# Kernel optimization log

Measured on AMD Instinct MI355X. Metric: run time of the kernel, lower is better.

Reference implementation:

```python
import jax, jax.numpy as jnp
import numpy as np

H = 256  # hidden_size


def setup_inputs() -> dict:
    key = jax.random.key(0)
    k1, k2, k3 = jax.random.split(key, 3)
    N, L, V, Emb = 128, 2048, 32000, 256
    X = jax.random.randint(k1, (N, L), 0, V, dtype=jnp.int64)
    E = jax.random.normal(k2, (V, Emb), dtype=jnp.float32) * 0.02
    W_w = jax.random.normal(k3, (4 * H, H + Emb), dtype=jnp.float32) * (1.0 / np.sqrt(H + Emb))
    W_b = jnp.zeros((4 * H,), dtype=jnp.float32)
    return {"X": X, "E": E, "W_w": W_w, "W_b": W_b}


def reference(X, E, W_w, W_b):
    # X: (N, L) int token ids
    N, L = X.shape
    Xe = E[X]                      # (N, L, Emb) embedded sequence
    Xe_t = jnp.swapaxes(Xe, 0, 1)  # (L, N, Emb) scan over time

    def step(carry, x_t):
        H_t, C_t = carry
        hx = jnp.concatenate([H_t, x_t], axis=1)           # (N, H+Emb)
        G = hx @ W_w.T + W_b                               # (N, 4H)
        F_g = jax.nn.sigmoid(G[:, :H])
        # NOTE: original code computes I = sigmoid(G[:, H:2H]) but never uses it
        O_g = jax.nn.sigmoid(G[:, 2 * H:3 * H])
        H_tmp = jnp.tanh(G[:, 3 * H:4 * H])
        # Faithful to source: C_t = F*C + O*H_tmp (uses O, not I)
        C_new = F_g * C_t + O_g * H_tmp
        H_new = O_g * jnp.tanh(C_new)
        return (H_new, C_new), None

    init = (jnp.zeros((N, H), Xe.dtype), jnp.zeros((N, H), Xe.dtype))
    (H_last, _), _ = jax.lax.scan(step, init, Xe_t)
    return H_last
```

## Files before the change

### kernel.cpp

```cpp
#include <hip/hip_runtime.h>
#include <hip/hip_bf16.h>

#define N_B   128
#define L_SEQ 2048
#define H_DIM 256
#define EMB   256
#define G3    768
#define G4    1024
#define WROW  512
#define V_SZ  32000


typedef unsigned short ushort_t;
typedef unsigned int   uint_t;

using f32x4  = __attribute__((ext_vector_type(4))) float;
using bf16x8 = __attribute__((ext_vector_type(8))) short;
using h2_t   = __attribute__((ext_vector_type(2))) _Float16;
using f16x8  = __attribute__((ext_vector_type(8))) _Float16;
using ushort4_t = __attribute__((ext_vector_type(4))) ushort_t;
using u32x4  = __attribute__((ext_vector_type(4))) uint_t;

__device__ __forceinline__ float bf2f(ushort_t u) {
  union { uint_t u; float f; } x; x.u = ((uint_t)u) << 16; return x.f;
}
__device__ __forceinline__ ushort_t f2bf(float f) {
  union { float f; uint_t u; } x; x.f = f;
  return (ushort_t)((x.u + 0x7fffu + ((x.u >> 16) & 1u)) >> 16);
}
__device__ __forceinline__ float rcp_f(float x) {
#if __has_builtin(__builtin_amdgcn_rcpf)
  return __builtin_amdgcn_rcpf(x);
#else
  return 1.0f / x;
#endif
}
__device__ __forceinline__ float clampf(float x, float lo, float hi) {
  return fminf(fmaxf(x, lo), hi);
}
__device__ __forceinline__ float sigmoid_f(float x) {
  x = clampf(x, -30.f, 30.f);
  return rcp_f(1.0f + __expf(-x));
}
__device__ __forceinline__ float tanh_f(float x) {
  x = clampf(x, -15.f, 15.f);
  float e = __expf(-2.0f * x);
  return (1.0f - e) * rcp_f(1.0f + e);
}
__device__ __forceinline__ h2_t bfpair_to_h2(uint_t u) {
  union { uint_t u; float f; } lo, hi;
  lo.u = u << 16;
  hi.u = u & 0xffff0000u;
  h2_t r; r.x = (_Float16)lo.f; r.y = (_Float16)hi.f; return r;
}

__device__ __forceinline__ int gmap(int g) { return (g < 256) ? g : g + 256; }

#define FENCE_V8(A) asm volatile("" :                                         \
  "+v"((A)[0]), "+v"((A)[1]), "+v"((A)[2]), "+v"((A)[3]),                     \
  "+v"((A)[4]), "+v"((A)[5]), "+v"((A)[6]), "+v"((A)[7]))

__global__ void dtype_probe(const uint_t* __restrict__ Ed,
                            const uint_t* __restrict__ Xd,
                            const uint_t* __restrict__ Wd,
                            uint_t* __restrict__ flags) {
  if (threadIdx.x != 0 || blockIdx.x != 0) return;
  int saneE = 0, saneW = 0;
  for (int i = 0; i < 256; ++i) {
    uint_t le = Ed[i] & 0xffffu, ee = (le >> 7) & 0xffu;
    if (ee == 0u || (ee >= 90u && ee <= 126u)) saneE++;
    uint_t lw = Wd[i] & 0xffffu, ew = (lw >> 7) & 0xffu;
    if (ew == 0u || (ew >= 90u && ew <= 126u)) saneW++;
  }
  uint_t nz = 0u;
  for (int i = 0; i < 128; ++i) nz |= Xd[2 * i + 1];
  flags[0] = (saneE < 192) ? 1u : 0u;
  flags[1] = (nz == 0u) ? 1u : 0u;
  flags[2] = (saneW < 192) ? 1u : 0u;
}

__global__ __launch_bounds__(256) void eg_gemm(const void* __restrict__ Ein,
                                               const void* __restrict__ Wwin,
                                               const void* __restrict__ Wbin,
                                               _Float16* __restrict__ Eg,
                                               const uint_t* __restrict__ flags) {
  __shared__ __align__(16) ushort_t At[16][264];
  const int tid = threadIdx.x;
  const int v0  = blockIdx.x * 16;
  const uint_t ef32 = flags[0];
  const uint_t wf32 = flags[2];

  if (!ef32) {
    const ushort_t* E = (const ushort_t*)Ein;
#pragma unroll
    for (int i = 0; i < 2; ++i) {
      int idx = tid + i * 256;
      int row = idx >> 5, seg = idx & 31;
      const uint4* src = (const uint4*)(E + (size_t)(v0 + row) * EMB + seg * 8);
      *(uint4*)&At[row][seg * 8] = *src;
    }
  } else {
    const float* Ef = (const float*)Ein;
#pragma unroll
    for (int i = 0; i < 4; ++i) {
      int idx = tid + i * 256;
      int row = idx >> 6, seg = idx & 63;
      float4 v = *(const float4*)(Ef + (size_t)(v0 + row) * EMB + seg * 4);
      ushort4_t s;
      s.x = f2bf(v.x); s.y = f2bf(v.y); s.z = f2bf(v.z); s.w = f2bf(v.w);
      *(ushort4_t*)&At[row][seg * 4] = s;
    }
  }
  __syncthreads();

  const int lane = tid & 63, wv = tid >> 6;
  const int m = lane & 15, q = lane >> 4;

  f32x4 acc[12];
#pragma unroll
  for (int nt = 0; nt < 12; ++nt) acc[nt] = f32x4{0.f, 0.f, 0.f, 0.f};

  if (!wf32) {
    const ushort_t* Ww = (const ushort_t*)Wwin;
#pragma unroll
    for (int kt = 0; kt < 8; ++kt) {
      bf16x8 a = *(const bf16x8*)&At[m][kt * 32 + q * 8];
#pragma unroll
      for (int nt = 0; nt < 12; ++nt) {
        int g  = wv * 192 + nt * 16 + m;
        int gr = gmap(g);
        const bf16x8* bp =
            (const bf16x8*)(Ww + (size_t)gr * WROW + EMB + kt * 32 + q * 8);
        acc[nt] = __builtin_amdgcn_mfma_f32_16x16x32_bf16(a, *bp, acc[nt], 0, 0, 0);
      }
    }
  } else {
    const float* Wf = (const float*)Wwin;
#pragma unroll
    for (int kt = 0; kt < 8; ++kt) {
      bf16x8 a = *(const bf16x8*)&At[m][kt * 32 + q * 8];
#pragma unroll
      for (int nt = 0; nt < 12; ++nt) {
        int g  = wv * 192 + nt * 16 + m;
        int gr = gmap(g);
        const float* wp = Wf + (size_t)gr * WROW + EMB + kt * 32 + q * 8;
        float4 w0 = *(const float4*)(wp);
        float4 w1 = *(const float4*)(wp + 4);
        bf16x8 b;
        b[0] = (short)f2bf(w0.x); b[1] = (short)f2bf(w0.y);
        b[2] = (short)f2bf(w0.z); b[3] = (short)f2bf(w0.w);
        b[4] = (short)f2bf(w1.x); b[5] = (short)f2bf(w1.y);
        b[6] = (short)f2bf(w1.z); b[7] = (short)f2bf(w1.w);
        acc[nt] = __builtin_amdgcn_mfma_f32_16x16x32_bf16(a, b, acc[nt], 0, 0, 0);
      }
    }
  }

#pragma unroll
  for (int nt = 0; nt < 12; ++nt) {
    int g  = wv * 192 + nt * 16 + m;
    int gr = gmap(g);
    float bias = wf32 ? ((const float*)Wbin)[gr] : bf2f(((const ushort_t*)Wbin)[gr]);
#pragma unroll
    for (int j = 0; j < 4; ++j) {
      int v = v0 + q * 4 + j;
      Eg[(size_t)v * G3 + g] = (_Float16)(acc[nt][j] + bias);
    }
  }
}

__global__ __launch_bounds__(512)
void lstm_rec_mfma(const int* __restrict__ Xi,
                   const void* __restrict__ Wwin,
                   const _Float16* __restrict__ Eg,
                   float* __restrict__ out,
                   const uint_t* __restrict__ flags) {
  __shared__ __align__(16) _Float16 hbuf[2][256];
  __shared__ __align__(16) float    Gbuf[G3];
  const int tid  = threadIdx.x;
  const int lane = tid & 63;
  const int w    = tid >> 6;
  const int q    = lane >> 4;
  const int rr   = lane & 15;
  const int n    = blockIdx.x;
  const uint_t wf32 = flags[2];
  const uint_t x64  = flags[1];

  u32x4 wAq[48];
  if (!wf32) {
    const ushort_t* Wb16 = (const ushort_t*)Wwin;
#pragma unroll
    for (int m = 0; m < 6; ++m) {
      const int grow = (w * 6 + m) * 16 + rr;
      const int wr   = gmap(grow);
      const ushort_t* rp = Wb16 + (size_t)wr * WROW + q * 8;
#pragma unroll
      for (int kt = 0; kt < 8; ++kt) {
        u32x4 v = *(const u32x4*)(rp + kt * 32);
        u32x4 t;
#pragma unroll
        for (int cc = 0; cc < 4; ++cc)
          t[cc] = __builtin_bit_cast(uint_t, bfpair_to_h2(v[cc]));
        wAq[m * 8 + kt] = t;
      }
    }
  } else {
    const float* Wf = (const float*)Wwin;
#pragma unroll
    for (int m = 0; m < 6; ++m) {
      const int grow = (w * 6 + m) * 16 + rr;
      const int wr   = gmap(grow);
      const float* rp = Wf + (size_t)wr * WROW + q * 8;
#pragma unroll
      for (int kt = 0; kt < 8; ++kt) {
        const float* pp = rp + kt * 32;
        float4 a = *(const float4*)(pp);
        float4 b = *(const float4*)(pp + 4);
        h2_t p0, p1, p2, p3;
        p0.x = (_Float16)a.x; p0.y = (_Float16)a.y;
        p1.x = (_Float16)a.z; p1.y = (_Float16)a.w;
        p2.x = (_Float16)b.x; p2.y = (_Float16)b.y;
        p3.x = (_Float16)b.z; p3.y = (_Float16)b.w;
        u32x4 t;
        t[0] = __builtin_bit_cast(uint_t, p0);
        t[1] = __builtin_bit_cast(uint_t, p1);
        t[2] = __builtin_bit_cast(uint_t, p2);
        t[3] = __builtin_bit_cast(uint_t, p3);
        wAq[m * 8 + kt] = t;
      }
    }
  }
  FENCE_V8(wAq);      FENCE_V8(wAq + 8);  FENCE_V8(wAq + 16);
  FENCE_V8(wAq + 24); FENCE_V8(wAq + 32); FENCE_V8(wAq + 40);

  if (tid < 256) hbuf[0][tid] = (_Float16)0.f;

  float c = 0.f, hlast = 0.f;
  const size_t xbase = (size_t)n * L_SEQ;

  float pxF = 0.f, pxO = 0.f, pxT = 0.f;
  if (tid < 256) {
    int tok0 = x64 ? Xi[xbase * 2] : Xi[xbase];
    if ((uint_t)tok0 >= (uint_t)V_SZ) tok0 = 0;
    const _Float16* e = Eg + (size_t)tok0 * G3 + tid;
    pxF = (float)e[0]; pxO = (float)e[256]; pxT = (float)e[512];
  }

  int cur = 0;
  for (int t = 0; t < L_SEQ; ++t) {
    __syncthreads();

    u32x4 bfq[8];
#pragma unroll
    for (int kt = 0; kt < 8; ++kt)
      bfq[kt] = *(const u32x4*)&hbuf[cur][kt * 32 + q * 8];

    float nF = 0.f, nO = 0.f, nT = 0.f;
    if (tid < 256) {
      int tp = (t + 1 < L_SEQ) ? (t + 1) : (L_SEQ - 1);
      int tok = x64 ? Xi[(xbase + tp) * 2] : Xi[xbase + tp];
      if ((uint_t)tok >= (uint_t)V_SZ) tok = 0;
      const _Float16* e = Eg + (size_t)tok * G3 + tid;
      nF = (float)e[0]; nO = (float)e[256]; nT = (float)e[512];
    }

    f32x4 acc[6];
#pragma unroll
    for (int m = 0; m < 6; ++m) acc[m] = f32x4{0.f, 0.f, 0.f, 0.f};
#pragma unroll
    for (int kt = 0; kt < 8; ++kt) {
      f16x8 b = __builtin_bit_cast(f16x8, bfq[kt]);
#pragma unroll
      for (int m = 0; m < 6; ++m) {
        f16x8 a = __builtin_bit_cast(f16x8, wAq[m * 8 + kt]);
        acc[m] = __builtin_amdgcn_mfma_f32_16x16x32_f16(a, b, acc[m], 0, 0, 0);
      }
    }

    if (rr == 0) {
#pragma unroll
      for (int m = 0; m < 6; ++m)
        *(f32x4*)&Gbuf[(w * 6 + m) * 16 + q * 4] = acc[m];
    }
    __syncthreads();

    if (tid < 256) {
      float aF = Gbuf[tid]       + pxF;
      float aO = Gbuf[256 + tid] + pxO;
      float aT = Gbuf[512 + tid] + pxT;
      float Fg = sigmoid_f(aF);
      float Og = sigmoid_f(aO);
      float Tg = tanh_f(aT);
      c = Fg * c + Og * Tg;
      float hv2 = Og * tanh_f(c);
      hlast = hv2;
      hbuf[cur ^ 1][tid] = (_Float16)hv2;
      pxF = nF; pxO = nO; pxT = nT;
    }
    cur ^= 1;
  }

  if (tid < 256) out[(size_t)n * H_DIM + tid] = hlast;
}

extern "C" void kernel_launch(void* const* d_in, const int* in_sizes, int n_in,
                              void* d_out, int out_size, void* d_ws, size_t ws_size,
                              hipStream_t stream) {
  const void* X  = d_in[0];
  const void* E  = d_in[1];
  const void* Ww = d_in[2];
  const void* Wb = d_in[3];
  for (int i = 0; i < n_in && i < 4; ++i) {
    switch (in_sizes[i]) {
      case N_B * L_SEQ: X  = d_in[i]; break;
      case V_SZ * EMB:  E  = d_in[i]; break;
      case G4 * WROW:   Ww = d_in[i]; break;
      case G4:          Wb = d_in[i]; break;
      default: break;
    }
  }
  float* out = (float*)d_out;

  uint_t*   flags = (uint_t*)d_ws;
  _Float16* Eg    = (_Float16*)((char*)d_ws + 256);

  dtype_probe<<<dim3(1), dim3(64), 0, stream>>>(
      (const uint_t*)E, (const uint_t*)X, (const uint_t*)Ww, flags);
  eg_gemm<<<dim3(V_SZ / 16), dim3(256), 0, stream>>>(E, Ww, Wb, Eg, flags);
  lstm_rec_mfma<<<dim3(N_B), dim3(512), 0, stream>>>(
      (const int*)X, Ww, Eg, out, flags);
}
```

Before: 3.360 ms.

## Split recurrent matvec across 16 waves with 3 row tiles each

```diff
diff --git a/kernel.cpp b/kernel.cpp
--- a/kernel.cpp
+++ b/kernel.cpp
@@ -169,7 +169,7 @@
   }
 }
 
-__global__ __launch_bounds__(512)
+__global__ __launch_bounds__(1024)
 void lstm_rec_mfma(const int* __restrict__ Xi,
                    const void* __restrict__ Wwin,
                    const _Float16* __restrict__ Eg,
@@ -186,12 +186,12 @@
   const uint_t wf32 = flags[2];
   const uint_t x64  = flags[1];
 
-  u32x4 wAq[48];
+  u32x4 wAq[24];
   if (!wf32) {
     const ushort_t* Wb16 = (const ushort_t*)Wwin;
 #pragma unroll
-    for (int m = 0; m < 6; ++m) {
-      const int grow = (w * 6 + m) * 16 + rr;
+    for (int m = 0; m < 3; ++m) {
+      const int grow = (w * 3 + m) * 16 + rr;
       const int wr   = gmap(grow);
       const ushort_t* rp = Wb16 + (size_t)wr * WROW + q * 8;
 #pragma unroll
@@ -207,8 +207,8 @@
   } else {
     const float* Wf = (const float*)Wwin;
 #pragma unroll
-    for (int m = 0; m < 6; ++m) {
-      const int grow = (w * 6 + m) * 16 + rr;
+    for (int m = 0; m < 3; ++m) {
+      const int grow = (w * 3 + m) * 16 + rr;
       const int wr   = gmap(grow);
       const float* rp = Wf + (size_t)wr * WROW + q * 8;
 #pragma unroll
@@ -230,8 +230,7 @@
       }
     }
   }
-  FENCE_V8(wAq);      FENCE_V8(wAq + 8);  FENCE_V8(wAq + 16);
-  FENCE_V8(wAq + 24); FENCE_V8(wAq + 32); FENCE_V8(wAq + 40);
+  FENCE_V8(wAq); FENCE_V8(wAq + 8); FENCE_V8(wAq + 16);
 
   if (tid < 256) hbuf[0][tid] = (_Float16)0.f;
 
@@ -249,11 +248,6 @@
   int cur = 0;
   for (int t = 0; t < L_SEQ; ++t) {
     __syncthreads();
-
-    u32x4 bfq[8];
-#pragma unroll
-    for (int kt = 0; kt < 8; ++kt)
-      bfq[kt] = *(const u32x4*)&hbuf[cur][kt * 32 + q * 8];
 
     float nF = 0.f, nO = 0.f, nT = 0.f;
     if (tid < 256) {
@@ -264,23 +258,24 @@
       nF = (float)e[0]; nO = (float)e[256]; nT = (float)e[512];
     }
 
-    f32x4 acc[6];
-#pragma unroll
-    for (int m = 0; m < 6; ++m) acc[m] = f32x4{0.f, 0.f, 0.f, 0.f};
+    f32x4 acc0 = f32x4{0.f, 0.f, 0.f, 0.f};
+    f32x4 acc1 = f32x4{0.f, 0.f, 0.f, 0.f};
+    f32x4 acc2 = f32x4{0.f, 0.f, 0.f, 0.f};
 #pragma unroll
     for (int kt = 0; kt < 8; ++kt) {
-      f16x8 b = __builtin_bit_cast(f16x8, bfq[kt]);
-#pragma unroll
-      for (int m = 0; m < 6; ++m) {
-        f16x8 a = __builtin_bit_cast(f16x8, wAq[m * 8 + kt]);
-        acc[m] = __builtin_amdgcn_mfma_f32_16x16x32_f16(a, b, acc[m], 0, 0, 0);
-      }
+      f16x8 b = *(const f16x8*)&hbuf[cur][kt * 32 + q * 8];
+      acc0 = __builtin_amdgcn_mfma_f32_16x16x32_f16(
+          __builtin_bit_cast(f16x8, wAq[kt]),      b, acc0, 0, 0, 0);
+      acc1 = __builtin_amdgcn_mfma_f32_16x16x32_f16(
+          __builtin_bit_cast(f16x8, wAq[8 + kt]),  b, acc1, 0, 0, 0);
+      acc2 = __builtin_amdgcn_mfma_f32_16x16x32_f16(
+          __builtin_bit_cast(f16x8, wAq[16 + kt]), b, acc2, 0, 0, 0);
     }
 
     if (rr == 0) {
-#pragma unroll
-      for (int m = 0; m < 6; ++m)
-        *(f32x4*)&Gbuf[(w * 6 + m) * 16 + q * 4] = acc[m];
+      *(f32x4*)&Gbuf[(w * 3 + 0) * 16 + q * 4] = acc0;
+      *(f32x4*)&Gbuf[(w * 3 + 1) * 16 + q * 4] = acc1;
+      *(f32x4*)&Gbuf[(w * 3 + 2) * 16 + q * 4] = acc2;
     }
     __syncthreads();
 
@@ -327,6 +322,6 @@
   dtype_probe<<<dim3(1), dim3(64), 0, stream>>>(
       (const uint_t*)E, (const uint_t*)X, (const uint_t*)Ww, flags);
   eg_gemm<<<dim3(V_SZ / 16), dim3(256), 0, stream>>>(E, Ww, Wb, Eg, flags);
-  lstm_rec_mfma<<<dim3(N_B), dim3(512), 0, stream>>>(
+  lstm_rec_mfma<<<dim3(N_B), dim3(1024), 0, stream>>>(
       (const int*)X, Ww, Eg, out, flags);
 }
```

Result: faster. 2.966 ms (-11.7%).
